# Kernel tuning notes

Hardware: AMD Instinct MI355X
Metric: run time of the kernel (lower is better)

The kernel has to match this reference:

```python
import jax, jax.numpy as jnp
import numpy as np


def _d2(a, b):
    # squared euclidean distances, clamped at 0 (matches _full_cdist before sqrt)
    a2 = jnp.sum(a * a, axis=1)[:, None]
    b2 = jnp.sum(b * b, axis=1)[None, :]
    return jnp.clip(a2 + b2 - 2.0 * (a @ b.T), 0.0, None)


def _node_weights(pts, w1, b1, w2, b2):
    h = jax.nn.relu(pts @ w1 + b1)
    logits = h @ w2 + b2
    w = jax.nn.softplus(logits) + 1e-6
    w = w / jnp.sum(w)
    return w[:, 0]


def setup_inputs() -> dict:
    key = jax.random.key(0)
    ks = jax.random.split(key, 8)
    N, M, D, H, S = 8192, 8192, 2, 32, 3
    return {
        "base_points": jax.random.normal(ks[0], (N, D), jnp.float32),
        "target_points": jax.random.normal(ks[1], (M, D), jnp.float32),
        "log_sigmas": jnp.log(jnp.array([0.05, 0.1, 0.2], jnp.float32)),
        "log_scale": 0.1 * jax.random.normal(ks[2], (D,), jnp.float32),
        "wn_w1": jax.random.normal(ks[3], (D, H), jnp.float32) / np.sqrt(D),
        "wn_b1": jnp.zeros((H,), jnp.float32),
        "wn_w2": jax.random.normal(ks[4], (H, 1), jnp.float32) / np.sqrt(H),
        "wn_b2": jnp.zeros((1,), jnp.float32),
        "g_w1": jax.random.normal(ks[5], (4, H), jnp.float32) / 2.0,
        "g_b1": jnp.zeros((H,), jnp.float32),
        "g_w2": jax.random.normal(ks[6], (H, S), jnp.float32) / np.sqrt(H),
        "g_b2": jnp.zeros((S,), jnp.float32),
        "bias": jnp.zeros((1,), jnp.float32),
    }


def reference(base_points, target_points, log_sigmas, log_scale,
              wn_w1, wn_b1, wn_w2, wn_b2,
              g_w1, g_b1, g_w2, g_b2, bias):
    # learned anisotropic per-axis scale
    scale = jnp.exp(log_scale)
    base = base_points * scale
    target = target_points * scale

    # learned positive, normalized node weights (shared weight_net)
    w_b = _node_weights(base, wn_w1, wn_b1, wn_w2, wn_b2)
    w_t = _node_weights(target, wn_w1, wn_b1, wn_w2, wn_b2)

    # kde_mmd_loss with center=True: subtract weighted mean of each cloud.
    bc = base - jnp.sum(w_b[:, None] * base, axis=0)
    tc = target - jnp.sum(w_t[:, None] * target, axis=0)

    # squared distances computed ONCE, reused across all sigma bands
    d2_aa = _d2(bc, bc)
    d2_bb = _d2(tc, tc)
    d2_ab = _d2(bc, tc)

    sigmas = jnp.exp(log_sigmas)

    def band_loss(sigma):
        inv = 1.0 / (2.0 * sigma * sigma)
        kaa = jnp.exp(-d2_aa * inv)
        kbb = jnp.exp(-d2_bb * inv)
        kab = jnp.exp(-d2_ab * inv)
        # weighted MMD^2: w_a K_aa w_a + w_b K_bb w_b - 2 w_a K_ab w_b
        return (w_b @ (kaa @ w_b) + w_t @ (kbb @ w_t)
                - 2.0 * (w_b @ (kab @ w_t)))

    per_band = jnp.stack([band_loss(sigmas[i]) for i in range(sigmas.shape[0])])

    # gating statistics (torch.tensor([...]) detaches -> stop_gradient)
    dist = jnp.sqrt(_d2(base, target))
    mean_dist = jnp.mean(dist)
    var_dist = jnp.var(dist, ddof=1)  # torch .var() is unbiased
    n_base = base_points.shape[0]
    size_diff = abs(float(n_base - target_points.shape[0])) / (n_base + 1e-6)
    weight_var = jnp.var(w_b, ddof=1) + jnp.var(w_t, ddof=1)
    stats = jax.lax.stop_gradient(
        jnp.stack([mean_dist, var_dist,
                   jnp.asarray(size_diff, base.dtype), weight_var]))

    mix_logits = jax.nn.relu(stats @ g_w1 + g_b1) @ g_w2 + g_b2
    gw = jax.nn.softplus(mix_logits)
    gw = gw / jnp.sum(gw)
    return jnp.sum(gw * per_band) + bias[0]
```

## Files before the change

### kernel.cpp

```cpp
#include <hip/hip_runtime.h>
#include <math.h>

#define JT 64
#define ITILE 1024
#define T8 8
#define NJOB_AB 1024
#define NJOB_TRI 576
#define NBLK (NJOB_AB + 2 * NJOB_TRI)
#define L2E 1.4426950408889634f

typedef float v2f __attribute__((ext_vector_type(2)));

__device__ inline float fexp2n(float x) {
  float r;
  asm("v_exp_f32 %0, -%1" : "=v"(r) : "v"(x));
  return r;
}
__device__ inline float fsqrt(float x) {
  float r;
  asm("v_sqrt_f32 %0, %1" : "=v"(r) : "v"(x));
  return r;
}

__device__ inline double wred_d(double v) {
#pragma unroll
  for (int o = 32; o > 0; o >>= 1) v += __shfl_down(v, o, 64);
  return v;
}

__device__ inline double bred(double v, double* sm) {
  v = wred_d(v);
  __syncthreads();
  if ((threadIdx.x & 63) == 0) sm[threadIdx.x >> 6] = v;
  __syncthreads();
  return sm[0] + sm[1] + sm[2] + sm[3];
}

__device__ inline void slot_reduce(const double* slot, double* smean) {
  if (threadIdx.x < 64) {
    int l = threadIdx.x;
    const double* sl = slot + l * 4;
#pragma unroll
    for (int c = 0; c < 4; ++c) {
      double v = sl[c];
      double vb = (l < 32) ? v : 0.0;
      double vt = (l < 32) ? 0.0 : v;
      vb = wred_d(vb);
      vt = wred_d(vt);
      if (l == 0) {
        smean[c] = vb;
        smean[4 + c] = vt;
      }
    }
  }
}

__global__ __launch_bounds__(256) void prep_kernel(
    const float* __restrict__ base, const float* __restrict__ target,
    const float* __restrict__ log_sigmas, const float* __restrict__ log_scale,
    const float* __restrict__ w1, const float* __restrict__ b1,
    const float* __restrict__ w2, const float* __restrict__ b2,
    float4* __restrict__ pxyu, double* __restrict__ slot,
    unsigned* __restrict__ fctr, int n) {
  __shared__ double sm[4];
  int gid = blockIdx.x * 256 + threadIdx.x;
  int isT = gid >= n;
  const float* pts = isT ? target : base;
  int idx = isT ? gid - n : gid;
  float ex = __expf(log_scale[0]);
  float ey = __expf(log_scale[1]);
  float s2 = __expf(log_sigmas[2]);
  float r2 = __fsqrt_rn(L2E / (2.f * s2 * s2));
  float2 p = ((const float2*)pts)[idx];
  float xr = p.x * ex, yr = p.y * ey;
  float logit = b2[0];
#pragma unroll
  for (int k = 0; k < 32; ++k) {
    float h = fmaf(xr, w1[k], fmaf(yr, w1[32 + k], b1[k]));
    h = fmaxf(h, 0.f);
    logit = fmaf(h, w2[k], logit);
  }
  float u = fmaxf(logit, 0.f) + log1pf(__expf(-fabsf(logit))) + 1e-6f;
  float X = xr * r2, Y = yr * r2;
  float q = fmaf(X, X, Y * Y);
  pxyu[gid] = make_float4(X, Y, q, u);
  double su = bred((double)u, sm);
  double qu = bred((double)u * (double)u, sm);
  double mx = bred((double)u * (double)X, sm);
  double my = bred((double)u * (double)Y, sm);
  if (threadIdx.x == 0) {
    double* s = slot + blockIdx.x * 4;
    s[0] = su;
    s[1] = qu;
    s[2] = mx;
    s[3] = my;
    if (blockIdx.x == 0) *fctr = 0u;
  }
}

template <bool AB, bool FAST>
__device__ inline void tile_loop(const float4* __restrict__ pJ4,
                                 const v2f xi2[2], const v2f yi2[2],
                                 const v2f Ai[2], const v2f al2[2], float cx2,
                                 float cy2, float rr0, float rr1, v2f a0[2],
                                 v2f a1[2], v2f a2[2], float& sdo,
                                 float& sqo) {
  v2f sd2 = {0.f, 0.f};
  v2f sq2 = {0.f, 0.f};
  const v2f vz = {0.f, 0.f};
#pragma unroll 4
  for (int j = 0; j < JT; ++j) {
    float4 J = pJ4[j];
    float xj = J.x, yj = J.y, qj = J.z, uj = J.w;
    float nbj;
    if constexpr (AB) nbj = -fmaf(cx2, xj, cy2 * yj);
#pragma unroll
    for (int g = 0; g < 2; ++g) {
      v2f c = Ai[g] + qj;
      v2f pos = c - xi2[g] * xj - yi2[g] * yj;
      v2f k2 = {fexp2n(pos.x), fexp2n(pos.y)};
      v2f k0, k1;
      if constexpr (FAST) {
        v2f t = k2 * k2;
        k1 = t * t;
        v2f t1 = k1 * k1;
        k0 = t1 * t1;
      } else {
        v2f m1 = pos * rr1;
        v2f m0 = pos * rr0;
        k1 = {fexp2n(m1.x), fexp2n(m1.y)};
        k0 = {fexp2n(m0.x), fexp2n(m0.y)};
      }
      a0[g] += uj * k0;
      a1[g] += uj * k1;
      a2[g] += uj * k2;
      if constexpr (AB) {
        v2f d2u = (pos + al2[g]) + nbj;
        d2u = __builtin_elementwise_max(d2u, vz);
        sq2 += d2u;
        v2f rt = {fsqrt(d2u.x), fsqrt(d2u.y)};
        sd2 += rt;
      }
    }
  }
  sdo = sd2.x + sd2.y;
  sqo = sq2.x + sq2.y;
}

__global__ __launch_bounds__(256) void pair_kernel(
    const float4* __restrict__ pxyu, const double* __restrict__ slot,
    double* __restrict__ paa, double* __restrict__ pbb,
    double* __restrict__ pab, double* __restrict__ psd,
    double* __restrict__ psq, unsigned* __restrict__ fctr,
    const float* __restrict__ log_sigmas, const float* __restrict__ g_w1,
    const float* __restrict__ g_b1, const float* __restrict__ g_w2,
    const float* __restrict__ g_b2, const float* __restrict__ bias,
    float* __restrict__ out, int n) {
  __shared__ double sm[4];
  __shared__ double smean[8];
  __shared__ int lastf;

  int b = blockIdx.x;
  int tid = threadIdx.x;
  int m, it, jt = 0, j0, pidx;
  if (b < NJOB_AB) {
    m = 2;
    pidx = b;
    it = b >> 7;
    j0 = (b & 127) * JT;
  } else {
    int r = b - NJOB_AB;
    m = (r < NJOB_TRI) ? 0 : 1;
    if (m == 1) r -= NJOB_TRI;
    pidx = r;
    int tile = r >> 4;
    int q = r & 15;
    int idx = tile, len = T8;
    it = 0;
    while (idx >= len) {
      idx -= len;
      --len;
      ++it;
    }
    jt = it + idx;
    j0 = jt * ITILE + q * JT;
  }
  const float4* pI = pxyu + ((m == 1) ? n : 0);
  const float4* pJ = pxyu + ((m == 0) ? 0 : n);

  float cx = 0.f, cy = 0.f, cx2 = 0.f, cy2 = 0.f, cc = 0.f;
  if (m == 2) {
    slot_reduce(slot, smean);
  }

  float s0 = __expf(log_sigmas[0]);
  float s1 = __expf(log_sigmas[1]);
  float s2 = __expf(log_sigmas[2]);
  float rr0 = (s2 * s2) / (s0 * s0);
  float rr1 = (s2 * s2) / (s1 * s1);
  bool fast = (fabsf(rr0 - 16.f) <= 0.016f) && (fabsf(rr1 - 4.f) <= 0.004f);

  if (m == 2) {
    __syncthreads();
    cx = (float)(smean[2] / smean[0] - smean[6] / smean[4]);
    cy = (float)(smean[3] / smean[0] - smean[7] / smean[4]);
    cx2 = 2.f * cx;
    cy2 = 2.f * cy;
    cc = cx * cx + cy * cy;
  }

  int i0 = it * ITILE + tid;
  v2f xi2[2], yi2[2], Ai[2], al2[2];
  float u[4];
#pragma unroll
  for (int i = 0; i < 4; ++i) {
    float4 P = pI[i0 + i * 256];
    u[i] = P.w;
    float xv = P.x, yv = P.y, alv = 0.f;
    float Av;
    if (m == 2) {
      xv -= cx;
      yv -= cy;
      alv = fmaf(cx2, xv, cy2 * yv) + cc;
      Av = fmaf(xv, xv, yv * yv);
    } else {
      Av = P.z;
    }
    int g = i >> 1, h = i & 1;
    xi2[g][h] = 2.f * xv;
    yi2[g][h] = 2.f * yv;
    Ai[g][h] = Av;
    al2[g][h] = alv;
  }

  v2f a0[2] = {}, a1[2] = {}, a2[2] = {};
  float sd = 0.f, sq = 0.f;
  const float4* pJ4 = pJ + j0;
  if (m == 2) {
    if (fast)
      tile_loop<true, true>(pJ4, xi2, yi2, Ai, al2, cx2, cy2, rr0, rr1, a0,
                            a1, a2, sd, sq);
    else
      tile_loop<true, false>(pJ4, xi2, yi2, Ai, al2, cx2, cy2, rr0, rr1, a0,
                             a1, a2, sd, sq);
  } else {
    if (fast)
      tile_loop<false, true>(pJ4, xi2, yi2, Ai, al2, cx2, cy2, rr0, rr1, a0,
                             a1, a2, sd, sq);
    else
      tile_loop<false, false>(pJ4, xi2, yi2, Ai, al2, cx2, cy2, rr0, rr1, a0,
                              a1, a2, sd, sq);
  }

  double wgt = (m != 2 && jt != it) ? 2.0 : 1.0;
  double c0 = 0.0, c1 = 0.0, c2 = 0.0;
#pragma unroll
  for (int i = 0; i < 4; ++i) {
    int g = i >> 1, h = i & 1;
    c0 += (double)u[i] * (double)a0[g][h];
    c1 += (double)u[i] * (double)a1[g][h];
    c2 += (double)u[i] * (double)a2[g][h];
  }
  double r0 = bred(c0, sm) * wgt;
  double r1 = bred(c1, sm) * wgt;
  double r2d = bred(c2, sm) * wgt;
  double* prow = (m == 0) ? paa : (m == 1) ? pbb : pab;
  int stride = (m == 2) ? NJOB_AB : NJOB_TRI;
  if (tid == 0) {
    prow[0 * stride + pidx] = r0;
    prow[1 * stride + pidx] = r1;
    prow[2 * stride + pidx] = r2d;
  }
  if (m == 2) {
    double rsd = bred((double)sd, sm);
    double rsq = bred((double)sq, sm);
    if (tid == 0) {
      psd[pidx] = rsd;
      psq[pidx] = rsq;
    }
  }

  if (tid == 0) {
    __threadfence();
    unsigned old = atomicAdd(fctr, 1u);
    lastf = (old == NBLK - 1) ? 1 : 0;
  }
  __syncthreads();
  if (!lastf) return;
  __threadfence();

  slot_reduce(slot, smean);
  __syncthreads();
  int t = tid;
  double vaa[3], vbb[3], vab[3];
  for (int s = 0; s < 3; ++s) {
    const double* pa = paa + s * NJOB_TRI;
    const double* pb = pbb + s * NJOB_TRI;
    const double* pc = pab + s * NJOB_AB;
    double va = pa[t] + pa[t + 256] + ((t < 64) ? pa[t + 512] : 0.0);
    double vb = pb[t] + pb[t + 256] + ((t < 64) ? pb[t + 512] : 0.0);
    double vc = pc[t] + pc[t + 256] + pc[t + 512] + pc[t + 768];
    vaa[s] = bred(va, sm);
    vbb[s] = bred(vb, sm);
    vab[s] = bred(vc, sm);
  }
  double sdt = bred(psd[t] + psd[t + 256] + psd[t + 512] + psd[t + 768], sm);
  double sqt = bred(psq[t] + psq[t + 256] + psq[t + 512] + psq[t + 768], sm);

  if (tid == 0) {
    double Sb = smean[0], Qb = smean[1], St = smean[4], Qt = smean[5];
    double pband[3];
    for (int s = 0; s < 3; ++s)
      pband[s] = vaa[s] / (Sb * Sb) + vbb[s] / (St * St) -
                 2.0 * vab[s] / (Sb * St);
    double s2d = (double)s2;
    double r2sq = (double)L2E / (2.0 * s2d * s2d);
    double sd_real = sdt / sqrt(r2sq);
    double sq_real = sqt / r2sq;
    double NN = (double)n;
    double NM = NN * NN;
    double mean_d = sd_real / NM;
    double var_d = (sq_real - sd_real * sd_real / NM) / (NM - 1.0);
    double wv = (Qb / (Sb * Sb) - 1.0 / NN) / (NN - 1.0) +
                (Qt / (St * St) - 1.0 / NN) / (NN - 1.0);
    float st[4] = {(float)mean_d, (float)var_d, 0.f, (float)wv};
    float gl[3] = {g_b2[0], g_b2[1], g_b2[2]};
    for (int k = 0; k < 32; ++k) {
      float h = g_b1[k];
      for (int c = 0; c < 4; ++c) h = fmaf(st[c], g_w1[c * 32 + k], h);
      h = fmaxf(h, 0.f);
      for (int s = 0; s < 3; ++s) gl[s] = fmaf(h, g_w2[k * 3 + s], gl[s]);
    }
    float gw[3];
    float gsum = 0.f;
    for (int s = 0; s < 3; ++s) {
      gw[s] = fmaxf(gl[s], 0.f) + log1pf(__expf(-fabsf(gl[s])));
      gsum += gw[s];
    }
    double r = 0.0;
    for (int s = 0; s < 3; ++s) r += (double)(gw[s] / gsum) * pband[s];
    out[0] = (float)(r + (double)bias[0]);
  }
}

extern "C" void kernel_launch(void* const* d_in, const int* in_sizes, int n_in,
                              void* d_out, int out_size, void* d_ws,
                              size_t ws_size, hipStream_t stream) {
  const float* base = (const float*)d_in[0];
  const float* target = (const float*)d_in[1];
  const float* log_sigmas = (const float*)d_in[2];
  const float* log_scale = (const float*)d_in[3];
  const float* wn_w1 = (const float*)d_in[4];
  const float* wn_b1 = (const float*)d_in[5];
  const float* wn_w2 = (const float*)d_in[6];
  const float* wn_b2 = (const float*)d_in[7];
  const float* g_w1 = (const float*)d_in[8];
  const float* g_b1 = (const float*)d_in[9];
  const float* g_w2 = (const float*)d_in[10];
  const float* g_b2 = (const float*)d_in[11];
  const float* bias = (const float*)d_in[12];
  int n = in_sizes[0] / 2;

  double* dbase = (double*)d_ws;
  double* slot = dbase;
  double* paa = dbase + 256;
  double* pbb = paa + 3 * NJOB_TRI;
  double* pab = pbb + 3 * NJOB_TRI;
  double* psd = pab + 3 * NJOB_AB;
  double* psq = psd + NJOB_AB;
  double* dend = psq + NJOB_AB;
  float4* pxyu = (float4*)dend;
  unsigned* fctr = (unsigned*)(pxyu + 2 * n);

  prep_kernel<<<(2 * n) / 256, 256, 0, stream>>>(
      base, target, log_sigmas, log_scale, wn_w1, wn_b1, wn_w2, wn_b2, pxyu,
      slot, fctr, n);
  pair_kernel<<<NBLK, 256, 0, stream>>>(pxyu, slot, paa, pbb, pab, psd, psq,
                                        fctr, log_sigmas, g_w1, g_b1, g_w2,
                                        g_b2, bias, (float*)d_out, n);
}
```

Baseline: 154.8 us.

## Compute sum of squared distances analytically and vectorize pair loop over j pairs

The sum of squared cross distances is now computed in closed form from per-cloud sums of x, y and x²+y² gathered in the prep kernel, so the per-pair accumulation of d² disappears. The j-tile is staged into LDS as separate x, y, u and bias arrays, and the inner loop packs two j values per v2f using explicit v_pk_add/mul/fma instructions across four i points. Distances are now formed as (xj-xi)²+(yj-yi)² rather than through a norm expansion. The closed-form variance risks cancellation error in double, and the inline asm may limit compiler scheduling.

```diff
diff --git a/kernel.cpp b/kernel.cpp
--- a/kernel.cpp
+++ b/kernel.cpp
@@ -21,6 +21,21 @@
   asm("v_sqrt_f32 %0, %1" : "=v"(r) : "v"(x));
   return r;
 }
+__device__ inline v2f pk_add(v2f a, v2f b) {
+  v2f d;
+  asm("v_pk_add_f32 %0, %1, %2" : "=v"(d) : "v"(a), "v"(b));
+  return d;
+}
+__device__ inline v2f pk_mul(v2f a, v2f b) {
+  v2f d;
+  asm("v_pk_mul_f32 %0, %1, %2" : "=v"(d) : "v"(a), "v"(b));
+  return d;
+}
+__device__ inline v2f pk_fma(v2f a, v2f b, v2f c) {
+  v2f d;
+  asm("v_pk_fma_f32 %0, %1, %2, %3" : "=v"(d) : "v"(a), "v"(b), "v"(c));
+  return d;
+}
 
 __device__ inline double wred_d(double v) {
 #pragma unroll
@@ -39,9 +54,9 @@
 __device__ inline void slot_reduce(const double* slot, double* smean) {
   if (threadIdx.x < 64) {
     int l = threadIdx.x;
-    const double* sl = slot + l * 4;
-#pragma unroll
-    for (int c = 0; c < 4; ++c) {
+    const double* sl = slot + l * 8;
+#pragma unroll
+    for (int c = 0; c < 7; ++c) {
       double v = sl[c];
       double vb = (l < 32) ? v : 0.0;
       double vt = (l < 32) ? 0.0 : v;
@@ -49,7 +64,7 @@
       vt = wred_d(vt);
       if (l == 0) {
         smean[c] = vb;
-        smean[4 + c] = vt;
+        smean[8 + c] = vt;
       }
     }
   }
@@ -88,76 +103,76 @@
   double qu = bred((double)u * (double)u, sm);
   double mx = bred((double)u * (double)X, sm);
   double my = bred((double)u * (double)Y, sm);
+  double sx = bred((double)X, sm);
+  double sy = bred((double)Y, sm);
+  double sq = bred((double)q, sm);
   if (threadIdx.x == 0) {
-    double* s = slot + blockIdx.x * 4;
+    double* s = slot + blockIdx.x * 8;
     s[0] = su;
     s[1] = qu;
     s[2] = mx;
     s[3] = my;
+    s[4] = sx;
+    s[5] = sy;
+    s[6] = sq;
     if (blockIdx.x == 0) *fctr = 0u;
   }
 }
 
-template <bool AB, bool FAST>
-__device__ inline void tile_loop(const float4* __restrict__ pJ4,
-                                 const v2f xi2[2], const v2f yi2[2],
-                                 const v2f Ai[2], const v2f al2[2], float cx2,
-                                 float cy2, float rr0, float rr1, v2f a0[2],
-                                 v2f a1[2], v2f a2[2], float& sdo,
-                                 float& sqo) {
-  v2f sd2 = {0.f, 0.f};
-  v2f sq2 = {0.f, 0.f};
-  const v2f vz = {0.f, 0.f};
-#pragma unroll 4
-  for (int j = 0; j < JT; ++j) {
-    float4 J = pJ4[j];
-    float xj = J.x, yj = J.y, qj = J.z, uj = J.w;
-    float nbj;
-    if constexpr (AB) nbj = -fmaf(cx2, xj, cy2 * yj);
-#pragma unroll
-    for (int g = 0; g < 2; ++g) {
-      v2f c = Ai[g] + qj;
-      v2f pos = c - xi2[g] * xj - yi2[g] * yj;
-      v2f k2 = {fexp2n(pos.x), fexp2n(pos.y)};
-      v2f k0, k1;
-      if constexpr (FAST) {
-        v2f t = k2 * k2;
-        k1 = t * t;
-        v2f t1 = k1 * k1;
-        k0 = t1 * t1;
-      } else {
-        v2f m1 = pos * rr1;
-        v2f m0 = pos * rr0;
-        k1 = {fexp2n(m1.x), fexp2n(m1.y)};
-        k0 = {fexp2n(m0.x), fexp2n(m0.y)};
+template <bool AB>
+__device__ inline void tile_loop_fast(const float* sx, const float* sy,
+                                      const float* su, const float* snb,
+                                      const v2f vnxi[4], const v2f vnyi[4],
+                                      const v2f vali[4], v2f a0[4], v2f a1[4],
+                                      v2f a2[4], float& sdo) {
+  float sdl = 0.f, sdh = 0.f;
+#pragma unroll 2
+  for (int jj = 0; jj < JT / 2; ++jj) {
+    v2f vxj = *(const v2f*)&sx[2 * jj];
+    v2f vyj = *(const v2f*)&sy[2 * jj];
+    v2f vuj = *(const v2f*)&su[2 * jj];
+    v2f vnbj;
+    if constexpr (AB) vnbj = *(const v2f*)&snb[2 * jj];
+#pragma unroll
+    for (int i = 0; i < 4; ++i) {
+      v2f dx = pk_add(vxj, vnxi[i]);
+      v2f dy = pk_add(vyj, vnyi[i]);
+      v2f t = pk_mul(dx, dx);
+      v2f pos = pk_fma(dy, dy, t);
+      float k2l = fexp2n(pos.x);
+      float k2h = fexp2n(pos.y);
+      v2f k2 = {k2l, k2h};
+      v2f t2 = pk_mul(k2, k2);
+      v2f k1 = pk_mul(t2, t2);
+      v2f t4 = pk_mul(k1, k1);
+      v2f k0 = pk_mul(t4, t4);
+      a0[i] = pk_fma(vuj, k0, a0[i]);
+      a1[i] = pk_fma(vuj, k1, a1[i]);
+      a2[i] = pk_fma(vuj, k2, a2[i]);
+      if constexpr (AB) {
+        v2f d2u = pk_add(pk_add(pos, vali[i]), vnbj);
+        sdl += fsqrt(fmaxf(d2u.x, 0.f));
+        sdh += fsqrt(fmaxf(d2u.y, 0.f));
       }
-      a0[g] += uj * k0;
-      a1[g] += uj * k1;
-      a2[g] += uj * k2;
-      if constexpr (AB) {
-        v2f d2u = (pos + al2[g]) + nbj;
-        d2u = __builtin_elementwise_max(d2u, vz);
-        sq2 += d2u;
-        v2f rt = {fsqrt(d2u.x), fsqrt(d2u.y)};
-        sd2 += rt;
-      }
-    }
-  }
-  sdo = sd2.x + sd2.y;
-  sqo = sq2.x + sq2.y;
+    }
+  }
+  sdo = sdl + sdh;
 }
 
 __global__ __launch_bounds__(256) void pair_kernel(
     const float4* __restrict__ pxyu, const double* __restrict__ slot,
     double* __restrict__ paa, double* __restrict__ pbb,
     double* __restrict__ pab, double* __restrict__ psd,
-    double* __restrict__ psq, unsigned* __restrict__ fctr,
-    const float* __restrict__ log_sigmas, const float* __restrict__ g_w1,
-    const float* __restrict__ g_b1, const float* __restrict__ g_w2,
-    const float* __restrict__ g_b2, const float* __restrict__ bias,
-    float* __restrict__ out, int n) {
+    unsigned* __restrict__ fctr, const float* __restrict__ log_sigmas,
+    const float* __restrict__ g_w1, const float* __restrict__ g_b1,
+    const float* __restrict__ g_w2, const float* __restrict__ g_b2,
+    const float* __restrict__ bias, float* __restrict__ out, int n) {
+  __shared__ __align__(16) float sx[JT];
+  __shared__ __align__(16) float sy[JT];
+  __shared__ __align__(16) float su[JT];
+  __shared__ __align__(16) float snb[JT];
   __shared__ double sm[4];
-  __shared__ double smean[8];
+  __shared__ double smean[16];
   __shared__ int lastf;
 
   int b = blockIdx.x;
@@ -202,64 +217,77 @@
 
   if (m == 2) {
     __syncthreads();
-    cx = (float)(smean[2] / smean[0] - smean[6] / smean[4]);
-    cy = (float)(smean[3] / smean[0] - smean[7] / smean[4]);
+    cx = (float)(smean[2] / smean[0] - smean[10] / smean[8]);
+    cy = (float)(smean[3] / smean[0] - smean[11] / smean[8]);
     cx2 = 2.f * cx;
     cy2 = 2.f * cy;
     cc = cx * cx + cy * cy;
   }
 
+  if (tid < JT) {
+    float4 v = pJ[j0 + tid];
+    sx[tid] = v.x;
+    sy[tid] = v.y;
+    su[tid] = v.w;
+    if (m == 2) snb[tid] = -fmaf(cx2, v.x, cy2 * v.y);
+  }
+  __syncthreads();
+
   int i0 = it * ITILE + tid;
-  v2f xi2[2], yi2[2], Ai[2], al2[2];
+  v2f vnxi[4], vnyi[4], vali[4];
   float u[4];
 #pragma unroll
   for (int i = 0; i < 4; ++i) {
     float4 P = pI[i0 + i * 256];
     u[i] = P.w;
     float xv = P.x, yv = P.y, alv = 0.f;
-    float Av;
     if (m == 2) {
       xv -= cx;
       yv -= cy;
       alv = fmaf(cx2, xv, cy2 * yv) + cc;
-      Av = fmaf(xv, xv, yv * yv);
-    } else {
-      Av = P.z;
-    }
-    int g = i >> 1, h = i & 1;
-    xi2[g][h] = 2.f * xv;
-    yi2[g][h] = 2.f * yv;
-    Ai[g][h] = Av;
-    al2[g][h] = alv;
-  }
-
-  v2f a0[2] = {}, a1[2] = {}, a2[2] = {};
-  float sd = 0.f, sq = 0.f;
-  const float4* pJ4 = pJ + j0;
-  if (m == 2) {
-    if (fast)
-      tile_loop<true, true>(pJ4, xi2, yi2, Ai, al2, cx2, cy2, rr0, rr1, a0,
-                            a1, a2, sd, sq);
+    }
+    vnxi[i] = (v2f){-xv, -xv};
+    vnyi[i] = (v2f){-yv, -yv};
+    vali[i] = (v2f){alv, alv};
+  }
+
+  v2f a0[4] = {}, a1[4] = {}, a2[4] = {};
+  float sd = 0.f;
+  if (fast) {
+    if (m == 2)
+      tile_loop_fast<true>(sx, sy, su, snb, vnxi, vnyi, vali, a0, a1, a2, sd);
     else
-      tile_loop<true, false>(pJ4, xi2, yi2, Ai, al2, cx2, cy2, rr0, rr1, a0,
-                             a1, a2, sd, sq);
+      tile_loop_fast<false>(sx, sy, su, snb, vnxi, vnyi, vali, a0, a1, a2,
+                            sd);
   } else {
-    if (fast)
-      tile_loop<false, true>(pJ4, xi2, yi2, Ai, al2, cx2, cy2, rr0, rr1, a0,
-                             a1, a2, sd, sq);
-    else
-      tile_loop<false, false>(pJ4, xi2, yi2, Ai, al2, cx2, cy2, rr0, rr1, a0,
-                              a1, a2, sd, sq);
+    for (int j = 0; j < JT; ++j) {
+      float xj = sx[j], yj = sy[j], uj = su[j];
+#pragma unroll
+      for (int i = 0; i < 4; ++i) {
+        float dx = xj + vnxi[i].x;
+        float dy = yj + vnyi[i].x;
+        float pos = fmaf(dx, dx, dy * dy);
+        float k2 = fexp2n(pos);
+        float k1 = fexp2n(pos * rr1);
+        float k0 = fexp2n(pos * rr0);
+        a0[i].x = fmaf(uj, k0, a0[i].x);
+        a1[i].x = fmaf(uj, k1, a1[i].x);
+        a2[i].x = fmaf(uj, k2, a2[i].x);
+        if (m == 2) {
+          float d2u = fmaxf(pos + vali[i].x + snb[j], 0.f);
+          sd += fsqrt(d2u);
+        }
+      }
+    }
   }
 
   double wgt = (m != 2 && jt != it) ? 2.0 : 1.0;
   double c0 = 0.0, c1 = 0.0, c2 = 0.0;
 #pragma unroll
   for (int i = 0; i < 4; ++i) {
-    int g = i >> 1, h = i & 1;
-    c0 += (double)u[i] * (double)a0[g][h];
-    c1 += (double)u[i] * (double)a1[g][h];
-    c2 += (double)u[i] * (double)a2[g][h];
+    c0 += (double)u[i] * (double)(a0[i].x + a0[i].y);
+    c1 += (double)u[i] * (double)(a1[i].x + a1[i].y);
+    c2 += (double)u[i] * (double)(a2[i].x + a2[i].y);
   }
   double r0 = bred(c0, sm) * wgt;
   double r1 = bred(c1, sm) * wgt;
@@ -273,11 +301,7 @@
   }
   if (m == 2) {
     double rsd = bred((double)sd, sm);
-    double rsq = bred((double)sq, sm);
-    if (tid == 0) {
-      psd[pidx] = rsd;
-      psq[pidx] = rsq;
-    }
+    if (tid == 0) psd[pidx] = rsd;
   }
 
   if (tid == 0) {
@@ -305,19 +329,21 @@
     vab[s] = bred(vc, sm);
   }
   double sdt = bred(psd[t] + psd[t + 256] + psd[t + 512] + psd[t + 768], sm);
-  double sqt = bred(psq[t] + psq[t + 256] + psq[t + 512] + psq[t + 768], sm);
 
   if (tid == 0) {
-    double Sb = smean[0], Qb = smean[1], St = smean[4], Qt = smean[5];
+    double Sb = smean[0], Qb = smean[1], St = smean[8], Qt = smean[9];
+    double SxB = smean[4], SyB = smean[5], SqB = smean[6];
+    double SxT = smean[12], SyT = smean[13], SqT = smean[14];
     double pband[3];
     for (int s = 0; s < 3; ++s)
       pband[s] = vaa[s] / (Sb * Sb) + vbb[s] / (St * St) -
                  2.0 * vab[s] / (Sb * St);
     double s2d = (double)s2;
     double r2sq = (double)L2E / (2.0 * s2d * s2d);
+    double NN = (double)n;
+    double sq_scaled = NN * (SqB + SqT) - 2.0 * (SxB * SxT + SyB * SyT);
     double sd_real = sdt / sqrt(r2sq);
-    double sq_real = sqt / r2sq;
-    double NN = (double)n;
+    double sq_real = sq_scaled / r2sq;
     double NM = NN * NN;
     double mean_d = sd_real / NM;
     double var_d = (sq_real - sd_real * sd_real / NM) / (NM - 1.0);
@@ -363,19 +389,18 @@
 
   double* dbase = (double*)d_ws;
   double* slot = dbase;
-  double* paa = dbase + 256;
+  double* paa = dbase + 512;
   double* pbb = paa + 3 * NJOB_TRI;
   double* pab = pbb + 3 * NJOB_TRI;
   double* psd = pab + 3 * NJOB_AB;
-  double* psq = psd + NJOB_AB;
-  double* dend = psq + NJOB_AB;
+  double* dend = psd + NJOB_AB;
   float4* pxyu = (float4*)dend;
   unsigned* fctr = (unsigned*)(pxyu + 2 * n);
 
   prep_kernel<<<(2 * n) / 256, 256, 0, stream>>>(
       base, target, log_sigmas, log_scale, wn_w1, wn_b1, wn_w2, wn_b2, pxyu,
       slot, fctr, n);
-  pair_kernel<<<NBLK, 256, 0, stream>>>(pxyu, slot, paa, pbb, pab, psd, psq,
-                                        fctr, log_sigmas, g_w1, g_b1, g_w2,
-                                        g_b2, bias, (float*)d_out, n);
-}
+  pair_kernel<<<NBLK, 256, 0, stream>>>(pxyu, slot, paa, pbb, pab, psd, fctr,
+                                        log_sigmas, g_w1, g_b1, g_w2, g_b2,
+                                        bias, (float*)d_out, n);
+}
```

Result: no change. 155.8 us (+0.6%).
